# Kernel optimization log

Measured on AMD Instinct MI355X. Metric: run time of the kernel, lower is better.

Reference implementation:

```python
import jax, jax.numpy as jnp
import numpy as np

B, LQ, LV = 32, 64, 128
QS, FS, BN = 512, 1024, 512

def setup_inputs() -> dict:
    key = jax.random.key(0)
    k1, k2, k3, k4, k5 = jax.random.split(key, 5)
    s = lambda n: 1.0 / np.sqrt(n)
    return {
        "phr_feats": jax.random.normal(k1, (B, LQ, QS), dtype=jnp.float32),
        "vis_feats": jax.random.normal(k2, (B, LV, FS), dtype=jnp.float32),
        "W": jax.random.uniform(k3, (BN, QS), jnp.float32, -s(QS), s(QS)),
        "U": jax.random.uniform(k4, (BN, FS), jnp.float32, -s(FS), s(FS)),
        "b": jnp.ones((BN,), dtype=jnp.float32),
        "w": jax.random.uniform(k5, (1, BN), jnp.float32, -s(BN), s(BN)),
    }

def reference(phr_feats, vis_feats, W, U, b, w):
    # Wh: [B,Lq,BN], Uv: [B,Lv,BN]
    Wh = jnp.einsum('bqd,nd->bqn', phr_feats, W)
    Uv = jnp.einsum('bvf,nf->bvn', vis_feats, U)
    # broadcast add + tanh: [B,Lq,Lv,BN]
    t = jnp.tanh(Wh[:, :, None, :] + Uv[:, None, :, :] + b)
    energies = jnp.einsum('bqvn,n->bqv', t, w[0])  # squeeze(-1)
    weights = jax.nn.softmax(energies, axis=2)
    aligned = jnp.einsum('bqv,bvf->bqf', weights, vis_feats)
    semantic_group_feats = jnp.concatenate([phr_feats, aligned], axis=2)
    return (semantic_group_feats, weights, energies)
```

## Files before the change

kernel.cpp:

```cpp
#include <hip/hip_runtime.h>

#define NB  32
#define NLQ 64
#define NLV 128
#define NQS 512
#define NFS 1024
#define NBN 512
#define CC  2.8853900817779268f

typedef float  floatx4 __attribute__((ext_vector_type(4)));
typedef __bf16 bf16x8  __attribute__((ext_vector_type(8)));
typedef unsigned short us;

__device__ __forceinline__ us f2bf(float f) {
    unsigned int u = __float_as_uint(f);
    u += 0x7fffu + ((u >> 16) & 1u);
    return (us)(u >> 16);
}
__device__ __forceinline__ unsigned int pktrunc(float lo, float hi) {
    return __builtin_amdgcn_perm(__float_as_uint(hi), __float_as_uint(lo), 0x07060302u);
}
__device__ __forceinline__ float blo(unsigned int u) {
    return __uint_as_float(u << 16);
}
__device__ __forceinline__ float bhi(unsigned int u) {
    return __uint_as_float(u & 0xffff0000u);
}

__device__ __forceinline__ void gemm64(
    us* As, us* Bs,
    const float* __restrict__ A, const float* __restrict__ Bt,
    const float* __restrict__ bias, us* __restrict__ C,
    int K, int bx, int by, int hasb)
{
    const int tid  = threadIdx.x;
    const int m0   = bx * 64;
    const int n0   = by * 64;
    const int wave = tid >> 6;
    const int lane = tid & 63;
    const int wm   = (wave >> 1) * 32;
    const int wn   = (wave & 1) * 32;
    const int srow = tid >> 2;
    const int sk   = (tid & 3) * 8;
    const int fm   = lane & 15;
    const int fko  = (lane >> 4) * 8;

    floatx4 acc[2][2] = {};
    const float* ag = A  + (size_t)(m0 + srow) * K + sk;
    const float* bg = Bt + (size_t)(n0 + srow) * K + sk;

    float4 a0 = *(const float4*)(ag),     a1 = *(const float4*)(ag + 4);
    float4 b0 = *(const float4*)(bg),     b1 = *(const float4*)(bg + 4);

    for (int k0 = 0; k0 < K; k0 += 32) {
        __syncthreads();
        uint4 av = { pktrunc(a0.x, a0.y), pktrunc(a0.z, a0.w),
                     pktrunc(a1.x, a1.y), pktrunc(a1.z, a1.w) };
        uint4 bv = { pktrunc(b0.x, b0.y), pktrunc(b0.z, b0.w),
                     pktrunc(b1.x, b1.y), pktrunc(b1.z, b1.w) };
        *(uint4*)(As + srow * 40 + sk) = av;
        *(uint4*)(Bs + srow * 40 + sk) = bv;
        const int kn = k0 + 32;
        if (kn < K) {
            a0 = *(const float4*)(ag + kn); a1 = *(const float4*)(ag + kn + 4);
            b0 = *(const float4*)(bg + kn); b1 = *(const float4*)(bg + kn + 4);
        }
        __syncthreads();
        bf16x8 am[2], bn[2];
        #pragma unroll
        for (int i = 0; i < 2; ++i)
            am[i] = *(const bf16x8*)(As + (wm + 16 * i + fm) * 40 + fko);
        #pragma unroll
        for (int j = 0; j < 2; ++j)
            bn[j] = *(const bf16x8*)(Bs + (wn + 16 * j + fm) * 40 + fko);
        #pragma unroll
        for (int i = 0; i < 2; ++i)
            #pragma unroll
            for (int j = 0; j < 2; ++j)
                acc[i][j] = __builtin_amdgcn_mfma_f32_16x16x32_bf16(am[i], bn[j], acc[i][j], 0, 0, 0);
    }

    const int cr = (lane >> 4) * 4;
    const int cc = lane & 15;
    #pragma unroll
    for (int i = 0; i < 2; ++i)
        #pragma unroll
        for (int j = 0; j < 2; ++j)
            #pragma unroll
            for (int r = 0; r < 4; ++r) {
                int gm = m0 + wm + 16 * i + cr + r;
                int gn = n0 + wn + 16 * j + cc;
                float v = acc[i][j][r];
                if (hasb) v += bias[gn];
                C[(size_t)gm * NBN + gn] = f2bf(__builtin_amdgcn_exp2f(CC * v));
            }
}

__global__ __launch_bounds__(256) void gemm_both(
    const float* __restrict__ phr, const float* __restrict__ W,
    const float* __restrict__ bias,
    const float* __restrict__ vis, const float* __restrict__ U,
    us* __restrict__ whY, us* __restrict__ uvY)
{
    __shared__ __align__(16) us As[64 * 40];
    __shared__ __align__(16) us Bs[64 * 40];
    int blk = blockIdx.x;
    if (blk < 256) {
        gemm64(As, Bs, phr, W, bias, whY, NQS, blk % 32, blk / 32, 1);
    } else {
        blk -= 256;
        gemm64(As, Bs, vis, U, bias, uvY, NFS, blk % 64, blk / 64, 0);
    }
}

__global__ __launch_bounds__(512, 4) void attn_fused(
    const us* __restrict__ whY,
    const us* __restrict__ uvY,
    const float* __restrict__ wvec,
    const float* __restrict__ phr,
    const float* __restrict__ vis,
    float* __restrict__ out_sgf, float* __restrict__ out_w, float* __restrict__ out_e)
{
    const float LOG2E = 1.4426950408889634f;
    const int blk  = blockIdx.x;
    const int b    = blk & 31;
    const int qg   = blk >> 5;
    const int tid  = threadIdx.x;
    const int wave = tid >> 6;
    const int lane = tid & 63;

    __shared__ float e_s[4][128];
    __shared__ float p_s[4][128];

    const int n0 = lane << 3;
    float Yq[4][8];
    #pragma unroll
    for (int qq = 0; qq < 4; ++qq) {
        uint4 y = *(const uint4*)(whY + (size_t)(b * NLQ + qg * 4 + qq) * NBN + n0);
        Yq[qq][0] = blo(y.x); Yq[qq][1] = bhi(y.x);
        Yq[qq][2] = blo(y.y); Yq[qq][3] = bhi(y.y);
        Yq[qq][4] = blo(y.z); Yq[qq][5] = bhi(y.z);
        Yq[qq][6] = blo(y.w); Yq[qq][7] = bhi(y.w);
    }
    float4 w0 = *(const float4*)(wvec + n0);
    float4 w1 = *(const float4*)(wvec + n0 + 4);
    float nw2[8] = { 2.f*w0.x, 2.f*w0.y, 2.f*w0.z, 2.f*w0.w,
                     2.f*w1.x, 2.f*w1.y, 2.f*w1.z, 2.f*w1.w };
    float sumw = w0.x + w0.y + w0.z + w0.w + w1.x + w1.y + w1.z + w1.w;
    #pragma unroll
    for (int off = 32; off; off >>= 1) sumw += __shfl_xor(sumw, off);

    #pragma unroll
    for (int vblk = 0; vblk < 2; ++vblk) {
        const us* base = uvY + ((size_t)b * NLV + wave * 16 + vblk * 8) * NBN + n0;
        float s[4][8];
        #pragma unroll
        for (int j = 0; j < 8; ++j) {
            uint4 u = *(const uint4*)(base + (size_t)j * NBN);
            float yv[8] = { blo(u.x), bhi(u.x), blo(u.y), bhi(u.y),
                            blo(u.z), bhi(u.z), blo(u.w), bhi(u.w) };
            #pragma unroll
            for (int qq = 0; qq < 4; ++qq) {
                float a = 0.f;
                #pragma unroll
                for (int k = 0; k < 8; ++k) {
                    float d = fmaf(yv[k], Yq[qq][k], 1.f);
                    a = fmaf(nw2[k], __builtin_amdgcn_rcpf(d), a);
                }
                s[qq][j] = a;
            }
        }
        #pragma unroll
        for (int qq = 0; qq < 4; ++qq) {
            #pragma unroll
            for (int m = 8; m <= 32; m <<= 1)
                #pragma unroll
                for (int j = 0; j < 8; ++j) s[qq][j] += __shfl_xor(s[qq][j], m);
            float t[4];
            #pragma unroll
            for (int p = 0; p < 4; ++p) {
                float ae = s[qq][2*p]     + __shfl_xor(s[qq][2*p],     1);
                float bo = s[qq][2*p + 1] + __shfl_xor(s[qq][2*p + 1], 1);
                t[p] = (lane & 1) ? bo : ae;
            }
            float u2[2];
            #pragma unroll
            for (int p = 0; p < 2; ++p) {
                float ae = t[2*p]     + __shfl_xor(t[2*p],     2);
                float bo = t[2*p + 1] + __shfl_xor(t[2*p + 1], 2);
                u2[p] = (lane & 2) ? bo : ae;
            }
            float ae = u2[0] + __shfl_xor(u2[0], 4);
            float bo = u2[1] + __shfl_xor(u2[1], 4);
            float r  = (lane & 4) ? bo : ae;
            if (lane < 8) e_s[qq][wave * 16 + vblk * 8 + lane] = sumw - r;
        }
    }
    __syncthreads();

    if (wave < 4) {
        const int q = wave;
        float e0 = e_s[q][lane];
        float e1 = e_s[q][lane + 64];
        float m = fmaxf(e0, e1);
        #pragma unroll
        for (int off = 32; off; off >>= 1) m = fmaxf(m, __shfl_xor(m, off));
        float x0 = __builtin_amdgcn_exp2f((e0 - m) * LOG2E);
        float x1 = __builtin_amdgcn_exp2f((e1 - m) * LOG2E);
        float ss = x0 + x1;
        #pragma unroll
        for (int off = 32; off; off >>= 1) ss += __shfl_xor(ss, off);
        float inv = __builtin_amdgcn_rcpf(ss);
        float p0 = x0 * inv, p1 = x1 * inv;
        size_t o = (size_t)(b * NLQ + qg * 4 + q) * NLV;
        out_w[o + lane]      = p0;
        out_w[o + lane + 64] = p1;
        out_e[o + lane]      = e0;
        out_e[o + lane + 64] = e1;
        p_s[q][lane]      = p0;
        p_s[q][lane + 64] = p1;
    } else {
        const int qq = wave - 4;
        const size_t r = (size_t)(b * NLQ + qg * 4 + qq);
        const float4* src = (const float4*)(phr + r * NQS);
        float4* dst = (float4*)(out_sgf + r * (NQS + NFS));
        dst[lane]      = src[lane];
        dst[lane + 64] = src[lane + 64];
    }
    __syncthreads();

    const int f0 = tid << 1;
    float2 acc[4] = {};
    const float* vb = vis + (size_t)b * NLV * NFS + f0;
    for (int v0 = 0; v0 < NLV; v0 += 4) {
        float4 pv[4];
        #pragma unroll
        for (int qq = 0; qq < 4; ++qq) pv[qq] = *(const float4*)&p_s[qq][v0];
        #pragma unroll
        for (int dv = 0; dv < 4; ++dv) {
            float2 x = *(const float2*)(vb + (size_t)(v0 + dv) * NFS);
            #pragma unroll
            for (int qq = 0; qq < 4; ++qq) {
                float p = (dv == 0) ? pv[qq].x : (dv == 1) ? pv[qq].y
                        : (dv == 2) ? pv[qq].z : pv[qq].w;
                acc[qq].x = fmaf(p, x.x, acc[qq].x);
                acc[qq].y = fmaf(p, x.y, acc[qq].y);
            }
        }
    }
    #pragma unroll
    for (int qq = 0; qq < 4; ++qq) {
        size_t row = (size_t)(b * NLQ + qg * 4 + qq);
        *(float2*)(out_sgf + row * (NQS + NFS) + NQS + f0) = acc[qq];
    }
}

extern "C" void kernel_launch(void* const* d_in, const int* in_sizes, int n_in,
                              void* d_out, int out_size, void* d_ws, size_t ws_size,
                              hipStream_t stream) {
    const float* phr  = (const float*)d_in[0];
    const float* vis  = (const float*)d_in[1];
    const float* W    = (const float*)d_in[2];
    const float* U    = (const float*)d_in[3];
    const float* bias = (const float*)d_in[4];
    const float* wvec = (const float*)d_in[5];

    char* ws = (char*)d_ws;
    us* whY = (us*)ws;
    us* uvY = (us*)(ws + (2u << 20));

    float* out     = (float*)d_out;
    float* out_sgf = out;
    float* out_w   = out_sgf + (size_t)NB * NLQ * (NQS + NFS);
    float* out_e   = out_w   + (size_t)NB * NLQ * NLV;

    gemm_both<<<768, 256, 0, stream>>>(phr, W, bias, vis, U, whY, uvY);
    attn_fused<<<NB * 16, 512, 0, stream>>>(whY, uvY, wvec, phr, vis,
                                            out_sgf, out_w, out_e);
}
```

Baseline: 128.8 us.

## Emit bf16 vis copy and phrase passthrough from GEMM; use bf16 vis in aggregation

The GEMM kernel's by==0 blocks now write the phrase features straight into the concatenated output and store a bf16-truncated copy of vis_feats into workspace, reusing loads they already perform. The attention kernel drops its phrase-copy branch and reads the bf16 vis copy for the weighted sum, halving the bytes read in that loop. The cost is lower precision for the aligned features (truncated, not rounded, bf16) and extra stores concentrated in a subset of GEMM blocks.

```diff
diff --git a/kernel.cpp b/kernel.cpp
--- a/kernel.cpp
+++ b/kernel.cpp
@@ -31,7 +31,8 @@
     us* As, us* Bs,
     const float* __restrict__ A, const float* __restrict__ Bt,
     const float* __restrict__ bias, us* __restrict__ C,
-    int K, int bx, int by, int hasb)
+    int K, int bx, int by, int hasb,
+    float* __restrict__ sgf, us* __restrict__ visb)
 {
     const int tid  = threadIdx.x;
     const int m0   = bx * 64;
@@ -54,10 +55,17 @@
 
     for (int k0 = 0; k0 < K; k0 += 32) {
         __syncthreads();
+        if (sgf) {
+            float* d = sgf + (size_t)(m0 + srow) * (NQS + NFS) + k0 + sk;
+            *(float4*)d       = a0;
+            *(float4*)(d + 4) = a1;
+        }
         uint4 av = { pktrunc(a0.x, a0.y), pktrunc(a0.z, a0.w),
                      pktrunc(a1.x, a1.y), pktrunc(a1.z, a1.w) };
         uint4 bv = { pktrunc(b0.x, b0.y), pktrunc(b0.z, b0.w),
                      pktrunc(b1.x, b1.y), pktrunc(b1.z, b1.w) };
+        if (visb)
+            *(uint4*)(visb + (size_t)(m0 + srow) * NFS + k0 + sk) = av;
         *(uint4*)(As + srow * 40 + sk) = av;
         *(uint4*)(Bs + srow * 40 + sk) = bv;
         const int kn = k0 + 32;
@@ -100,16 +108,21 @@
     const float* __restrict__ phr, const float* __restrict__ W,
     const float* __restrict__ bias,
     const float* __restrict__ vis, const float* __restrict__ U,
-    us* __restrict__ whY, us* __restrict__ uvY)
+    us* __restrict__ whY, us* __restrict__ uvY,
+    float* __restrict__ out_sgf, us* __restrict__ vis_b)
 {
     __shared__ __align__(16) us As[64 * 40];
     __shared__ __align__(16) us Bs[64 * 40];
     int blk = blockIdx.x;
     if (blk < 256) {
-        gemm64(As, Bs, phr, W, bias, whY, NQS, blk % 32, blk / 32, 1);
+        int bx = blk % 32, by = blk / 32;
+        gemm64(As, Bs, phr, W, bias, whY, NQS, bx, by, 1,
+               by == 0 ? out_sgf : nullptr, nullptr);
     } else {
         blk -= 256;
-        gemm64(As, Bs, vis, U, bias, uvY, NFS, blk % 64, blk / 64, 0);
+        int bx = blk % 64, by = blk / 64;
+        gemm64(As, Bs, vis, U, bias, uvY, NFS, bx, by, 0,
+               nullptr, by == 0 ? vis_b : nullptr);
     }
 }
 
@@ -117,8 +130,7 @@
     const us* __restrict__ whY,
     const us* __restrict__ uvY,
     const float* __restrict__ wvec,
-    const float* __restrict__ phr,
-    const float* __restrict__ vis,
+    const us* __restrict__ vis_b,
     float* __restrict__ out_sgf, float* __restrict__ out_w, float* __restrict__ out_e)
 {
     const float LOG2E = 1.4426950408889634f;
@@ -219,32 +231,26 @@
         out_e[o + lane + 64] = e1;
         p_s[q][lane]      = p0;
         p_s[q][lane + 64] = p1;
-    } else {
-        const int qq = wave - 4;
-        const size_t r = (size_t)(b * NLQ + qg * 4 + qq);
-        const float4* src = (const float4*)(phr + r * NQS);
-        float4* dst = (float4*)(out_sgf + r * (NQS + NFS));
-        dst[lane]      = src[lane];
-        dst[lane + 64] = src[lane + 64];
     }
     __syncthreads();
 
     const int f0 = tid << 1;
     float2 acc[4] = {};
-    const float* vb = vis + (size_t)b * NLV * NFS + f0;
+    const us* vb = vis_b + (size_t)b * NLV * NFS + f0;
     for (int v0 = 0; v0 < NLV; v0 += 4) {
         float4 pv[4];
         #pragma unroll
         for (int qq = 0; qq < 4; ++qq) pv[qq] = *(const float4*)&p_s[qq][v0];
         #pragma unroll
         for (int dv = 0; dv < 4; ++dv) {
-            float2 x = *(const float2*)(vb + (size_t)(v0 + dv) * NFS);
+            unsigned int u = *(const unsigned int*)(vb + (size_t)(v0 + dv) * NFS);
+            float x0 = blo(u), x1 = bhi(u);
             #pragma unroll
             for (int qq = 0; qq < 4; ++qq) {
                 float p = (dv == 0) ? pv[qq].x : (dv == 1) ? pv[qq].y
                         : (dv == 2) ? pv[qq].z : pv[qq].w;
-                acc[qq].x = fmaf(p, x.x, acc[qq].x);
-                acc[qq].y = fmaf(p, x.y, acc[qq].y);
+                acc[qq].x = fmaf(p, x0, acc[qq].x);
+                acc[qq].y = fmaf(p, x1, acc[qq].y);
             }
         }
     }
@@ -266,15 +272,17 @@
     const float* wvec = (const float*)d_in[5];
 
     char* ws = (char*)d_ws;
-    us* whY = (us*)ws;
-    us* uvY = (us*)(ws + (2u << 20));
+    us* whY   = (us*)ws;
+    us* uvY   = (us*)(ws + (2u << 20));
+    us* vis_b = (us*)(ws + (6u << 20));
 
     float* out     = (float*)d_out;
     float* out_sgf = out;
     float* out_w   = out_sgf + (size_t)NB * NLQ * (NQS + NFS);
     float* out_e   = out_w   + (size_t)NB * NLQ * NLV;
 
-    gemm_both<<<768, 256, 0, stream>>>(phr, W, bias, vis, U, whY, uvY);
-    attn_fused<<<NB * 16, 512, 0, stream>>>(whY, uvY, wvec, phr, vis,
+    gemm_both<<<768, 256, 0, stream>>>(phr, W, bias, vis, U, whY, uvY,
+                                       out_sgf, vis_b);
+    attn_fused<<<NB * 16, 512, 0, stream>>>(whY, uvY, wvec, vis_b,
                                             out_sgf, out_w, out_e);
 }
```

Result: slower. 140.8 us (+9.3%).
